# Optimization experiments

Measured on AMD Instinct MI355X. Metric: run time of the kernel, lower is better.

Reference implementation:

```python
import jax, jax.numpy as jnp
import numpy as np
import math

N_FREQ = 128
D_EMB = 64
SLOT_DIM = 256
MLP_HIDDEN = 1024
B, N_SLOTS, N_FEAT = 32, 128, 4096
SIN_DIM = 1 + 2 * N_FREQ
EPS_LN = 1e-5


def _lin_init(key, dout, din):
    k1, k2 = jax.random.split(key)
    s = 1.0 / np.sqrt(din)
    w = jax.random.uniform(k1, (dout, din), minval=-s, maxval=s, dtype=jnp.float32)
    b = jax.random.uniform(k2, (dout,), minval=-s, maxval=s, dtype=jnp.float32)
    return w, b


def setup_inputs() -> dict:
    key = jax.random.key(0)
    ks = jax.random.split(key, 20)
    inp = {}
    # four TimeDepWeight heads: (prefix, d_out, d_in)
    heads = [("q", SLOT_DIM, SLOT_DIM), ("g", SLOT_DIM, 2 * SLOT_DIM),
             ("f0", MLP_HIDDEN, 2 * SLOT_DIM), ("f1", SLOT_DIM, MLP_HIDDEN)]
    i = 0
    for name, dout, din in heads:
        w0, b0 = _lin_init(ks[i], D_EMB, SIN_DIM)
        w1, b1 = _lin_init(ks[i + 1], D_EMB, D_EMB)
        wp, bp = _lin_init(ks[i + 2], dout * din, D_EMB)
        i += 3
        inp[f"{name}_w0"], inp[f"{name}_b0"] = w0, b0
        inp[f"{name}_w1"], inp[f"{name}_b1"] = w1, b1
        inp[f"{name}_wp"], inp[f"{name}_bp"] = wp, bp
    # LayerNorm affine params (eqx.nn.LayerNorm defaults: weight=1, bias=0)
    inp["lnA_w"] = jnp.ones((SLOT_DIM,), jnp.float32)
    inp["lnA_b"] = jnp.zeros((SLOT_DIM,), jnp.float32)
    inp["lnF_w"] = jnp.ones((SLOT_DIM,), jnp.float32)
    inp["lnF_b"] = jnp.zeros((SLOT_DIM,), jnp.float32)
    inp["t"] = jax.random.uniform(ks[12], (1,), dtype=jnp.float32)
    inp["slots"] = jax.random.normal(ks[13], (B, N_SLOTS, SLOT_DIM), jnp.float32)
    inp["k"] = jax.random.normal(ks[14], (B, N_FEAT, SLOT_DIM), jnp.float32)
    inp["v"] = jax.random.normal(ks[15], (B, N_FEAT, SLOT_DIM), jnp.float32)
    return inp


def _tdw(t, w0, b0, w1, b1, wp, bp, d_out, d_in):
    # Sinusoidal(t) -> 2-layer SiLU MLP -> proj -> [d_out, d_in]
    freqs = (-math.log(10000.0) / N_FREQ) * jnp.arange(N_FREQ, dtype=jnp.float32)
    wt = freqs * t
    emb = jnp.concatenate([t[None], jnp.sin(wt), jnp.cos(wt)])
    h = jax.nn.silu(w0 @ emb + b0)
    h = jax.nn.silu(w1 @ h + b1)
    return (wp @ h + bp).reshape(d_out, d_in)


def _layernorm(x, w, b):
    mu = x.mean(-1, keepdims=True)
    var = ((x - mu) ** 2).mean(-1, keepdims=True)
    return (x - mu) / jnp.sqrt(var + EPS_LN) * w + b


def reference(t, slots, k, v,
              q_w0, q_b0, q_w1, q_b1, q_wp, q_bp,
              g_w0, g_b0, g_w1, g_b1, g_wp, g_bp,
              f0_w0, f0_b0, f0_w1, f0_b1, f0_wp, f0_bp,
              f1_w0, f1_b0, f1_w1, f1_b1, f1_wp, f1_bp,
              lnA_w, lnA_b, lnF_w, lnF_b):
    ts = t[0]
    scale = SLOT_DIM ** (-0.5)
    W_q = _tdw(ts, q_w0, q_b0, q_w1, q_b1, q_wp, q_bp, SLOT_DIM, SLOT_DIM)
    W_gate = _tdw(ts, g_w0, g_b0, g_w1, g_b1, g_wp, g_bp, SLOT_DIM, 2 * SLOT_DIM)
    W_ff0 = _tdw(ts, f0_w0, f0_b0, f0_w1, f0_b1, f0_wp, f0_bp, MLP_HIDDEN, 2 * SLOT_DIM)
    W_ff1 = _tdw(ts, f1_w0, f1_b0, f1_w1, f1_b1, f1_wp, f1_bp, SLOT_DIM, MLP_HIDDEN)

    slots_norm = _layernorm(slots, lnA_w, lnA_b)                  # [B,N,D]
    q = jnp.einsum('bnd,od->bno', slots_norm, W_q)                # [B,N,D]
    att_logits = jnp.einsum('bnd,bmd->bnm', q, k) * scale         # [B,N,M]
    att = jax.nn.softmax(att_logits, axis=1)                      # over slots
    att = att / (att.sum(axis=-1, keepdims=True) + 1e-08)         # renorm over feats
    f_attn = jnp.einsum('bnm,bmd->bnd', att, v)                   # [B,N,D]

    gate_input = jnp.concatenate([slots_norm, f_attn], axis=-1)   # [B,N,2D]
    gate = jax.nn.sigmoid(jnp.einsum('bnd,od->bno', gate_input, W_gate))

    slots_ff = _layernorm(slots, lnF_w, lnF_b)
    ff_input = jnp.concatenate([slots_ff, f_attn], axis=-1)       # [B,N,2D]
    h = jax.nn.relu(jnp.einsum('bnd,od->bno', ff_input, W_ff0))   # [B,N,H]
    g_ff = jnp.einsum('bnd,od->bno', h, W_ff1)                    # [B,N,D]
    return gate * f_attn + g_ff
```

## Files before the change

kernel.cpp:

```cpp
#include <hip/hip_runtime.h>
#include <hip/hip_bf16.h>
#include <cstdint>

typedef unsigned short u16;
typedef unsigned int u32;
typedef __attribute__((ext_vector_type(8))) short short8;
typedef __attribute__((ext_vector_type(4))) float f32x4;

#define TID ((int)threadIdx.x)

__device__ __forceinline__ float b2f(u16 u) { return __uint_as_float(((u32)u) << 16); }
__device__ __forceinline__ u16 f2b(float f) {
    u32 u = __float_as_uint(f);
    u += 0x7fffu + ((u >> 16) & 1u);
    return (u16)(u >> 16);
}
__device__ __forceinline__ float2 upk(u32 u) {
    float2 r;
    r.x = __uint_as_float(u << 16);
    r.y = __uint_as_float(u & 0xffff0000u);
    return r;
}
__device__ __forceinline__ float silu_f(float x) { return x / (1.f + __expf(-x)); }

__device__ __forceinline__ float ldx(const void* p, size_t i, bool bf) {
    float v;
    if (bf) v = b2f(((const u16*)p)[i]);
    else    v = ((const float*)p)[i];
    return v;
}

#define BB 32
#define NN 128
#define DD 256
#define MM 4096
#define HH 1024
#define BN (BB * NN)

#define O_FLAG 0
#define O_H2   8
#define O_S    (O_H2 + 256)
#define O_FAT  (O_S + BN)
#define O_WQT  (O_FAT + BN * DD)
#define O_WGT  (O_WQT + 256 * 256)
#define O_WF0T (O_WGT + 512 * 256)
#define O_WF1T (O_WF0T + 512 * 1024)
#define O_SNA  (O_WF1T + 1024 * 256)
#define O_SNF  (O_SNA + BN * DD)
#define O_Q    (O_SNF + BN * DD)
#define O_H    (O_Q + BN * DD)

__global__ void probe_dtype(const void* lnAw, int* flag) {
    u32 bits = *(const u32*)lnAw;
    *flag = ((bits & 0xFFFFu) == 0x3F80u) ? 1 : 0;
}

__global__ __launch_bounds__(256) void tdw_mlp(
    const void* t,
    const void* qw0, const void* qb0, const void* qw1, const void* qb1,
    const void* gw0, const void* gb0, const void* gw1, const void* gb1,
    const void* f0w0, const void* f0b0, const void* f0w1, const void* f0b1,
    const void* f1w0, const void* f1b0, const void* f1w1, const void* f1b1,
    float* h2out, const int* flagp)
{
    __shared__ float emb[257];
    __shared__ float h1s[256];
    bool bf = (*flagp != 0);
    float tv = ldx(t, 0, bf);
    const float c = -9.210340371976184f / 128.f;
    for (int i = TID; i < 257; i += 256) {
        float val;
        if (i == 0) val = tv;
        else if (i <= 128) val = sinf(c * (float)(i - 1) * tv);
        else val = cosf(c * (float)(i - 129) * tv);
        emb[i] = val;
    }
    __syncthreads();
    int head = TID >> 6, o = TID & 63;
    const void* w0s[4] = {qw0, gw0, f0w0, f1w0};
    const void* b0s[4] = {qb0, gb0, f0b0, f1b0};
    const void* w1s[4] = {qw1, gw1, f0w1, f1w1};
    const void* b1s[4] = {qb1, gb1, f0b1, f1b1};
    float acc = ldx(b0s[head], o, bf);
    if (bf) {
        const u16* w0 = (const u16*)w0s[head];
        for (int j = 0; j < 257; j++) acc += b2f(w0[o * 257 + j]) * emb[j];
    } else {
        const float* w0 = (const float*)w0s[head];
        for (int j = 0; j < 257; j++) acc += w0[o * 257 + j] * emb[j];
    }
    h1s[TID] = silu_f(acc);
    __syncthreads();
    float acc2 = ldx(b1s[head], o, bf);
    if (bf) {
        const u16* w1 = (const u16*)w1s[head];
        for (int j = 0; j < 64; j++) acc2 += b2f(w1[o * 64 + j]) * h1s[head * 64 + j];
    } else {
        const float* w1 = (const float*)w1s[head];
        for (int j = 0; j < 64; j++) acc2 += w1[o * 64 + j] * h1s[head * 64 + j];
    }
    h2out[TID] = silu_f(acc2);
}

__global__ __launch_bounds__(256) void tdw_proj(
    const void* __restrict__ wp, const void* __restrict__ bp,
    const float* __restrict__ h2, float* __restrict__ WT,
    int dout_shift, int din, const int* flagp)
{
    __shared__ float h2s[64];
    bool bf = (*flagp != 0);
    if (TID < 64) h2s[TID] = h2[TID];
    __syncthreads();
    int j = blockIdx.x * 256 + TID;
    int d = j >> dout_shift;
    int o = j & ((1 << dout_shift) - 1);
    long i = (long)o * din + d;
    float acc;
    if (bf) acc = b2f(((const u16*)bp)[i]);
    else    acc = ((const float*)bp)[i];
    if (bf) {
        const uint4* row = (const uint4*)((const u16*)wp + i * 64);
#pragma unroll
        for (int r = 0; r < 8; r++) {
            uint4 u = row[r];
            float2 p;
            p = upk(u.x); acc += p.x * h2s[r * 8 + 0] + p.y * h2s[r * 8 + 1];
            p = upk(u.y); acc += p.x * h2s[r * 8 + 2] + p.y * h2s[r * 8 + 3];
            p = upk(u.z); acc += p.x * h2s[r * 8 + 4] + p.y * h2s[r * 8 + 5];
            p = upk(u.w); acc += p.x * h2s[r * 8 + 6] + p.y * h2s[r * 8 + 7];
        }
    } else {
        const float4* row = (const float4*)((const float*)wp + i * 64);
#pragma unroll
        for (int r = 0; r < 16; r++) {
            float4 u = row[r];
            acc += u.x * h2s[r * 4 + 0] + u.y * h2s[r * 4 + 1]
                 + u.z * h2s[r * 4 + 2] + u.w * h2s[r * 4 + 3];
        }
    }
    WT[j] = acc;
}

__global__ __launch_bounds__(256) void layernorm_k(
    const void* __restrict__ slots,
    const void* lnAw, const void* lnAb, const void* lnFw, const void* lnFb,
    float* __restrict__ snA, float* __restrict__ snF, const int* flagp)
{
    int bn = blockIdx.x;
    bool bf = (*flagp != 0);
    float x;
    if (bf) x = b2f(((const u16*)slots)[(size_t)bn * DD + TID]);
    else    x = ((const float*)slots)[(size_t)bn * DD + TID];
    float s1 = x, s2 = x * x;
    for (int off = 32; off; off >>= 1) {
        s1 += __shfl_down(s1, off, 64);
        s2 += __shfl_down(s2, off, 64);
    }
    __shared__ float r1[4], r2[4];
    __shared__ float mu_s, rs_s;
    if ((TID & 63) == 0) { r1[TID >> 6] = s1; r2[TID >> 6] = s2; }
    __syncthreads();
    if (TID == 0) {
        float a = r1[0] + r1[1] + r1[2] + r1[3];
        float b = r2[0] + r2[1] + r2[2] + r2[3];
        float mu = a * (1.f / 256.f);
        float var = b * (1.f / 256.f) - mu * mu;
        mu_s = mu;
        rs_s = rsqrtf(var + 1e-5f);
    }
    __syncthreads();
    float xh = (x - mu_s) * rs_s;
    snA[(size_t)bn * DD + TID] = xh * ldx(lnAw, TID, bf) + ldx(lnAb, TID, bf);
    snF[(size_t)bn * DD + TID] = xh * ldx(lnFw, TID, bf) + ldx(lnFb, TID, bf);
}

__global__ __launch_bounds__(256) void qproj(
    const float* __restrict__ snA, const float* __restrict__ WqT, u16* __restrict__ qb)
{
    int rb = blockIdx.x;
    __shared__ float sn[8][256];
    for (int idx = TID; idx < 2048; idx += 256)
        sn[idx >> 8][idx & 255] = snA[(size_t)rb * 2048 + idx];
    __syncthreads();
    float acc[8] = {0, 0, 0, 0, 0, 0, 0, 0};
    for (int d = 0; d < 256; d++) {
        float w = WqT[d * 256 + TID];
#pragma unroll
        for (int r = 0; r < 8; r++) acc[r] += sn[r][d] * w;
    }
    for (int r = 0; r < 8; r++) qb[(size_t)(rb * 8 + r) * 256 + TID] = f2b(acc[r]);
}

__global__ __launch_bounds__(256, 2) void attn_mfma(
    const u16* __restrict__ qbG,
    const void* __restrict__ k, const void* __restrict__ v,
    float* __restrict__ fat, float* __restrict__ S, const int* flagp)
{
    const int b = blockIdx.y;
    const int m0 = blockIdx.x * 128;
    const bool bf = (*flagp != 0);
    const int t = TID;
    const int l = t & 63, w = t >> 6;
    const int lg = l >> 4;
    const int ll = l & 15;

    __shared__ alignas(16) u16 AB[128 * 128];
    __shared__ alignas(16) u16 vt[256 * 40];

    u16* qb = AB;
    u16* kb = AB + 8192;

    f32x4 acc[2][8];
#pragma unroll
    for (int s = 0; s < 2; s++)
#pragma unroll
        for (int nt = 0; nt < 8; nt++) acc[s][nt] = {0.f, 0.f, 0.f, 0.f};

    for (int dc = 0; dc < 4; dc++) {
        {
            const u32* qg = (const u32*)qbG + (size_t)b * 128 * 128 + dc * 32;
#pragma unroll
            for (int i = 0; i < 16; i++) {
                int fid = i * 256 + t;
                int n = fid >> 5, dp = fid & 31;
                u32 val = qg[n * 128 + dp];
                *(u32*)((char*)qb + n * 128 + ((dp * 4) ^ ((n & 7) << 4))) = val;
            }
        }
        if (bf) {
            const u32* kg = (const u32*)k + ((size_t)(b * MM + m0)) * 128 + dc * 32;
#pragma unroll
            for (int i = 0; i < 16; i++) {
                int fid = i * 256 + t;
                int mm = fid >> 5, dp = fid & 31;
                u32 val = kg[(size_t)mm * 128 + dp];
                *(u32*)((char*)kb + mm * 128 + ((dp * 4) ^ ((mm & 7) << 4))) = val;
            }
        } else {
            const float4* kg = (const float4*)k + ((size_t)(b * MM + m0)) * 64 + dc * 16;
#pragma unroll
            for (int i = 0; i < 8; i++) {
                int fid = i * 256 + t;
                int mm = fid >> 4, q4 = fid & 15;
                float4 f = kg[(size_t)mm * 64 + q4];
                u32 p0 = ((u32)f2b(f.x)) | ((u32)f2b(f.y) << 16);
                u32 p1 = ((u32)f2b(f.z)) | ((u32)f2b(f.w) << 16);
                char* base = (char*)kb + mm * 128;
                *(u32*)(base + (((q4 * 8) + 0) ^ ((mm & 7) << 4))) = p0;
                *(u32*)(base + (((q4 * 8) + 4) ^ ((mm & 7) << 4))) = p1;
            }
        }
        __syncthreads();
#pragma unroll
        for (int ds = 0; ds < 2; ds++) {
            int doff = ds * 64 + lg * 16;
            short8 bfr[2];
#pragma unroll
            for (int s = 0; s < 2; s++) {
                int mm = w * 32 + s * 16 + ll;
                bfr[s] = *(const short8*)((char*)kb + mm * 128 + (doff ^ ((mm & 7) << 4)));
            }
#pragma unroll
            for (int nt = 0; nt < 8; nt++) {
                int n = nt * 16 + ll;
                short8 af = *(const short8*)((char*)qb + n * 128 + (doff ^ ((n & 7) << 4)));
                acc[0][nt] = __builtin_amdgcn_mfma_f32_16x16x32_bf16(af, bfr[0], acc[0][nt], 0, 0, 0);
                acc[1][nt] = __builtin_amdgcn_mfma_f32_16x16x32_bf16(af, bfr[1], acc[1][nt], 0, 0, 0);
            }
        }
        __syncthreads();
    }

    const float scale = 0.0625f;
#pragma unroll
    for (int s = 0; s < 2; s++) {
        float cm = -1e30f;
#pragma unroll
        for (int nt = 0; nt < 8; nt++)
#pragma unroll
            for (int r = 0; r < 4; r++) cm = fmaxf(cm, acc[s][nt][r]);
        cm = fmaxf(cm, __shfl_xor(cm, 16));
        cm = fmaxf(cm, __shfl_xor(cm, 32));
        float cs = 0.f;
#pragma unroll
        for (int nt = 0; nt < 8; nt++)
#pragma unroll
            for (int r = 0; r < 4; r++) {
                float ev = __expf((acc[s][nt][r] - cm) * scale);
                acc[s][nt][r] = ev;
                cs += ev;
            }
        cs += __shfl_xor(cs, 16);
        cs += __shfl_xor(cs, 32);
        float inv = 1.f / cs;
#pragma unroll
        for (int nt = 0; nt < 8; nt++)
#pragma unroll
            for (int r = 0; r < 4; r++) acc[s][nt][r] *= inv;
    }

    u16* att = AB;
#pragma unroll
    for (int s = 0; s < 2; s++)
#pragma unroll
        for (int nt = 0; nt < 8; nt++)
#pragma unroll
            for (int r = 0; r < 4; r++) {
                int n = nt * 16 + lg * 4 + r;
                int mw = w * 32 + s * 16 + ll;
                *(u16*)((char*)att + n * 256 + ((mw * 2) ^ ((n & 7) << 4))) = f2b(acc[s][nt][r]);
            }
#pragma unroll
    for (int nt = 0; nt < 8; nt++)
#pragma unroll
        for (int r = 0; r < 4; r++) {
            float vsum = acc[0][nt][r] + acc[1][nt][r];
            vsum += __shfl_xor(vsum, 1);
            vsum += __shfl_xor(vsum, 2);
            vsum += __shfl_xor(vsum, 4);
            vsum += __shfl_xor(vsum, 8);
            if (ll == 0) atomicAdd(S + b * NN + nt * 16 + lg * 4 + r, vsum);
        }

    f32x4 accp[8][4];
#pragma unroll
    for (int nt = 0; nt < 8; nt++)
#pragma unroll
        for (int dt = 0; dt < 4; dt++) accp[nt][dt] = {0.f, 0.f, 0.f, 0.f};

    for (int ms = 0; ms < 4; ms++) {
        if (bf) {
            const u32* vg = (const u32*)v + ((size_t)(b * MM + m0 + ms * 32)) * 128;
#pragma unroll
            for (int i = 0; i < 16; i++) {
                int fid = i * 256 + t;
                int mm = fid >> 7, du = fid & 127;
                u32 val = vg[(size_t)mm * 128 + du];
                vt[(du * 2 + 0) * 40 + mm] = (u16)(val & 0xffffu);
                vt[(du * 2 + 1) * 40 + mm] = (u16)(val >> 16);
            }
        } else {
            const float4* vg = (const float4*)v + ((size_t)(b * MM + m0 + ms * 32)) * 64;
#pragma unroll
            for (int i = 0; i < 8; i++) {
                int fid = i * 256 + t;
                int mm = fid >> 6, q4 = fid & 63;
                float4 f = vg[(size_t)mm * 64 + q4];
                vt[(q4 * 4 + 0) * 40 + mm] = f2b(f.x);
                vt[(q4 * 4 + 1) * 40 + mm] = f2b(f.y);
                vt[(q4 * 4 + 2) * 40 + mm] = f2b(f.z);
                vt[(q4 * 4 + 3) * 40 + mm] = f2b(f.w);
            }
        }
        __syncthreads();
        short8 bfr[4];
#pragma unroll
        for (int dt = 0; dt < 4; dt++) {
            int dv = w * 64 + dt * 16 + ll;
            bfr[dt] = *(const short8*)(vt + dv * 40 + lg * 8);
        }
#pragma unroll
        for (int nt = 0; nt < 8; nt++) {
            int n = nt * 16 + ll;
            short8 af = *(const short8*)((char*)att + n * 256 + ((ms * 64 + lg * 16) ^ ((n & 7) << 4)));
#pragma unroll
            for (int dt = 0; dt < 4; dt++)
                accp[nt][dt] = __builtin_amdgcn_mfma_f32_16x16x32_bf16(af, bfr[dt], accp[nt][dt], 0, 0, 0);
        }
        __syncthreads();
    }

    float* fb = fat + ((size_t)b * NN) * DD;
#pragma unroll
    for (int nt = 0; nt < 8; nt++)
#pragma unroll
        for (int dt = 0; dt < 4; dt++)
#pragma unroll
            for (int r = 0; r < 4; r++) {
                int n = nt * 16 + lg * 4 + r;
                int dv = w * 64 + dt * 16 + ll;
                atomicAdd(fb + (size_t)n * DD + dv, accp[nt][dt][r]);
            }
}

__global__ __launch_bounds__(256) void ffa(
    const float* __restrict__ snF, const float* __restrict__ fat, const float* __restrict__ S,
    const float* __restrict__ Wf0T, float* __restrict__ h)
{
    int rb = blockIdx.x;
    __shared__ float fi[8][512];
    __shared__ float rsh[8];
    if (TID < 8) rsh[TID] = 1.f / (S[rb * 8 + TID] + 1e-8f);
    __syncthreads();
    for (int idx = TID; idx < 4096; idx += 256) {
        int r = idx >> 9, dd = idx & 511;
        int bn = rb * 8 + r;
        fi[r][dd] = (dd < 256) ? snF[(size_t)bn * 256 + dd]
                               : fat[(size_t)bn * 256 + dd - 256] * rsh[r];
    }
    __syncthreads();
    float acc[8][4] = {};
    for (int d = 0; d < 512; d++) {
        float w0 = Wf0T[d * 1024 + TID];
        float w1 = Wf0T[d * 1024 + TID + 256];
        float w2 = Wf0T[d * 1024 + TID + 512];
        float w3 = Wf0T[d * 1024 + TID + 768];
#pragma unroll
        for (int r = 0; r < 8; r++) {
            float f = fi[r][d];
            acc[r][0] = fmaf(f, w0, acc[r][0]);
            acc[r][1] = fmaf(f, w1, acc[r][1]);
            acc[r][2] = fmaf(f, w2, acc[r][2]);
            acc[r][3] = fmaf(f, w3, acc[r][3]);
        }
    }
    for (int r = 0; r < 8; r++) {
        size_t base = (size_t)(rb * 8 + r) * 1024;
        h[base + TID] = fmaxf(acc[r][0], 0.f);
        h[base + TID + 256] = fmaxf(acc[r][1], 0.f);
        h[base + TID + 512] = fmaxf(acc[r][2], 0.f);
        h[base + TID + 768] = fmaxf(acc[r][3], 0.f);
    }
}

__global__ __launch_bounds__(256) void ffb(
    const float* __restrict__ snA, const float* __restrict__ fat, const float* __restrict__ S,
    const float* __restrict__ WgT, const float* __restrict__ Wf1T,
    const float* __restrict__ h, void* __restrict__ out, const int* flagp)
{
    int rb = blockIdx.x;
    bool bf = (*flagp != 0);
    __shared__ float gi[8][512];
    __shared__ float hs[8][1024];
    __shared__ float rsh[8];
    if (TID < 8) rsh[TID] = 1.f / (S[rb * 8 + TID] + 1e-8f);
    __syncthreads();
    for (int idx = TID; idx < 4096; idx += 256) {
        int r = idx >> 9, dd = idx & 511;
        int bn = rb * 8 + r;
        gi[r][dd] = (dd < 256) ? snA[(size_t)bn * 256 + dd]
                               : fat[(size_t)bn * 256 + dd - 256] * rsh[r];
    }
    for (int idx = TID; idx < 8192; idx += 256) {
        int r = idx >> 10, dd = idx & 1023;
        hs[r][dd] = h[(size_t)(rb * 8 + r) * 1024 + dd];
    }
    __syncthreads();
    float ag[8] = {0, 0, 0, 0, 0, 0, 0, 0};
    float af[8] = {0, 0, 0, 0, 0, 0, 0, 0};
    for (int d = 0; d < 512; d++) {
        float w = WgT[d * 256 + TID];
#pragma unroll
        for (int r = 0; r < 8; r++) ag[r] = fmaf(gi[r][d], w, ag[r]);
    }
    for (int j = 0; j < 1024; j++) {
        float w = Wf1T[j * 256 + TID];
#pragma unroll
        for (int r = 0; r < 8; r++) af[r] = fmaf(hs[r][j], w, af[r]);
    }
    for (int r = 0; r < 8; r++) {
        int bn = rb * 8 + r;
        float fa = gi[r][256 + TID];
        float g = 1.f / (1.f + __expf(-ag[r]));
        float val = g * fa + af[r];
        if (bf) ((u16*)out)[(size_t)bn * 256 + TID] = f2b(val);
        else    ((float*)out)[(size_t)bn * 256 + TID] = val;
    }
}

extern "C" void kernel_launch(void* const* d_in, const int* in_sizes, int n_in,
                              void* d_out, int out_size, void* d_ws, size_t ws_size,
                              hipStream_t stream)
{
    const void* in[32];
    bool sig_order = (n_in >= 1 && in_sizes[0] == 1);
    for (int i = 0; i < 32; i++) {
        int j = sig_order ? ((i < 28) ? (i + 4) : (i - 28)) : i;
        in[i] = d_in[j];
    }

    const void* qw0 = in[0];  const void* qb0 = in[1];
    const void* qw1 = in[2];  const void* qb1 = in[3];
    const void* qwp = in[4];  const void* qbp = in[5];
    const void* gw0 = in[6];  const void* gb0 = in[7];
    const void* gw1 = in[8];  const void* gb1 = in[9];
    const void* gwp = in[10]; const void* gbp = in[11];
    const void* f0w0 = in[12]; const void* f0b0 = in[13];
    const void* f0w1 = in[14]; const void* f0b1 = in[15];
    const void* f0wp = in[16]; const void* f0bp = in[17];
    const void* f1w0 = in[18]; const void* f1b0 = in[19];
    const void* f1w1 = in[20]; const void* f1b1 = in[21];
    const void* f1wp = in[22]; const void* f1bp = in[23];
    const void* lnAw = in[24]; const void* lnAb = in[25];
    const void* lnFw = in[26]; const void* lnFb = in[27];
    const void* t    = in[28]; const void* slots = in[29];
    const void* kk   = in[30]; const void* vv   = in[31];

    float* F = (float*)d_ws;
    int* flagp = (int*)(F + O_FLAG);

    hipMemsetAsync(F + O_S, 0, (size_t)(BN + BN * DD) * sizeof(float), stream);

    probe_dtype<<<1, 1, 0, stream>>>(lnAw, flagp);

    tdw_mlp<<<1, 256, 0, stream>>>(t, qw0, qb0, qw1, qb1, gw0, gb0, gw1, gb1,
                                   f0w0, f0b0, f0w1, f0b1, f1w0, f1b0, f1w1, f1b1,
                                   F + O_H2, flagp);

    tdw_proj<<<256, 256, 0, stream>>>(qwp, qbp, F + O_H2 + 0, F + O_WQT, 8, 256, flagp);
    tdw_proj<<<512, 256, 0, stream>>>(gwp, gbp, F + O_H2 + 64, F + O_WGT, 8, 512, flagp);
    tdw_proj<<<2048, 256, 0, stream>>>(f0wp, f0bp, F + O_H2 + 128, F + O_WF0T, 10, 512, flagp);
    tdw_proj<<<1024, 256, 0, stream>>>(f1wp, f1bp, F + O_H2 + 192, F + O_WF1T, 8, 1024, flagp);

    layernorm_k<<<BN, 256, 0, stream>>>(slots, lnAw, lnAb, lnFw, lnFb,
                                        F + O_SNA, F + O_SNF, flagp);

    qproj<<<BN / 8, 256, 0, stream>>>(F + O_SNA, F + O_WQT, (u16*)(F + O_Q));

    attn_mfma<<<dim3(MM / 128, BB), 256, 0, stream>>>((const u16*)(F + O_Q), kk, vv,
                                                      F + O_FAT, F + O_S, flagp);

    ffa<<<BN / 8, 256, 0, stream>>>(F + O_SNF, F + O_FAT, F + O_S, F + O_WF0T, F + O_H);

    ffb<<<BN / 8, 256, 0, stream>>>(F + O_SNA, F + O_FAT, F + O_S, F + O_WGT, F + O_WF1T,
                                    F + O_H, d_out, flagp);
}
```

Before: 1.132 ms.

## Replace attention atomics with per-tile partials plus reduction; vectorize FFN smem loads

The attention kernel now writes each M-tile's partial f_attn to its own slice of workspace instead of doing float atomicAdd into one buffer, and a new reduce_fat kernel sums the 32 partials. The memset of the fat buffer is dropped accordingly. The qproj, ffa and ffb kernels load into shared memory with float4 and unroll their inner loops by 4 so shared-memory reads are vectorized. The partial buffer adds 32x the f_attn size in extra writes and reads, which trades atomic contention for bandwidth. It also reuses the workspace at O_H, which ffa later overwrites with h, so the ordering matters.

```diff
diff --git a/kernel.cpp b/kernel.cpp
--- a/kernel.cpp
+++ b/kernel.cpp
@@ -49,6 +49,7 @@
 #define O_SNF  (O_SNA + BN * DD)
 #define O_Q    (O_SNF + BN * DD)
 #define O_H    (O_Q + BN * DD)
+#define O_FATP O_H
 
 __global__ void probe_dtype(const void* lnAw, int* flag) {
     u32 bits = *(const u32*)lnAw;
@@ -179,14 +180,22 @@
 {
     int rb = blockIdx.x;
     __shared__ float sn[8][256];
-    for (int idx = TID; idx < 2048; idx += 256)
-        sn[idx >> 8][idx & 255] = snA[(size_t)rb * 2048 + idx];
+    for (int idx = TID; idx < 512; idx += 256) {
+        int r = idx >> 6, q4 = idx & 63;
+        *(float4*)&sn[r][q4 * 4] = *(const float4*)(snA + (size_t)rb * 2048 + r * 256 + q4 * 4);
+    }
     __syncthreads();
     float acc[8] = {0, 0, 0, 0, 0, 0, 0, 0};
-    for (int d = 0; d < 256; d++) {
-        float w = WqT[d * 256 + TID];
-#pragma unroll
-        for (int r = 0; r < 8; r++) acc[r] += sn[r][d] * w;
+    for (int d = 0; d < 256; d += 4) {
+        float w0 = WqT[(d + 0) * 256 + TID];
+        float w1 = WqT[(d + 1) * 256 + TID];
+        float w2 = WqT[(d + 2) * 256 + TID];
+        float w3 = WqT[(d + 3) * 256 + TID];
+#pragma unroll
+        for (int r = 0; r < 8; r++) {
+            float4 s4 = *(const float4*)&sn[r][d];
+            acc[r] = fmaf(s4.x, w0, fmaf(s4.y, w1, fmaf(s4.z, w2, fmaf(s4.w, w3, acc[r]))));
+        }
     }
     for (int r = 0; r < 8; r++) qb[(size_t)(rb * 8 + r) * 256 + TID] = f2b(acc[r]);
 }
@@ -194,10 +203,11 @@
 __global__ __launch_bounds__(256, 2) void attn_mfma(
     const u16* __restrict__ qbG,
     const void* __restrict__ k, const void* __restrict__ v,
-    float* __restrict__ fat, float* __restrict__ S, const int* flagp)
+    float* __restrict__ fatP, float* __restrict__ S, const int* flagp)
 {
     const int b = blockIdx.y;
-    const int m0 = blockIdx.x * 128;
+    const int mt = blockIdx.x;
+    const int m0 = mt * 128;
     const bool bf = (*flagp != 0);
     const int t = TID;
     const int l = t & 63, w = t >> 6;
@@ -370,7 +380,7 @@
         __syncthreads();
     }
 
-    float* fb = fat + ((size_t)b * NN) * DD;
+    float* fp = fatP + ((size_t)mt * BN + (size_t)b * NN) * DD;
 #pragma unroll
     for (int nt = 0; nt < 8; nt++)
 #pragma unroll
@@ -379,8 +389,21 @@
             for (int r = 0; r < 4; r++) {
                 int n = nt * 16 + lg * 4 + r;
                 int dv = w * 64 + dt * 16 + ll;
-                atomicAdd(fb + (size_t)n * DD + dv, accp[nt][dt][r]);
-            }
+                fp[(size_t)n * DD + dv] = accp[nt][dt][r];
+            }
+}
+
+__global__ __launch_bounds__(256) void reduce_fat(
+    const float* __restrict__ fatP, float* __restrict__ fat)
+{
+    size_t i = ((size_t)blockIdx.x * 256 + TID) * 4;
+    float4 a = *(const float4*)(fatP + i);
+#pragma unroll
+    for (int mt = 1; mt < 32; mt++) {
+        float4 bb = *(const float4*)(fatP + (size_t)mt * (size_t)BN * DD + i);
+        a.x += bb.x; a.y += bb.y; a.z += bb.z; a.w += bb.w;
+    }
+    *(float4*)(fat + i) = a;
 }
 
 __global__ __launch_bounds__(256) void ffa(
@@ -392,26 +415,37 @@
     __shared__ float rsh[8];
     if (TID < 8) rsh[TID] = 1.f / (S[rb * 8 + TID] + 1e-8f);
     __syncthreads();
-    for (int idx = TID; idx < 4096; idx += 256) {
-        int r = idx >> 9, dd = idx & 511;
-        int bn = rb * 8 + r;
-        fi[r][dd] = (dd < 256) ? snF[(size_t)bn * 256 + dd]
-                               : fat[(size_t)bn * 256 + dd - 256] * rsh[r];
+    for (int idx = TID; idx < 1024; idx += 256) {
+        int r = idx >> 7, q4 = idx & 127;
+        size_t bn = (size_t)rb * 8 + r;
+        float4 val;
+        if (q4 < 64) val = *(const float4*)(snF + bn * 256 + q4 * 4);
+        else {
+            val = *(const float4*)(fat + bn * 256 + (q4 - 64) * 4);
+            float s = rsh[r];
+            val.x *= s; val.y *= s; val.z *= s; val.w *= s;
+        }
+        *(float4*)&fi[r][q4 * 4] = val;
     }
     __syncthreads();
     float acc[8][4] = {};
-    for (int d = 0; d < 512; d++) {
-        float w0 = Wf0T[d * 1024 + TID];
-        float w1 = Wf0T[d * 1024 + TID + 256];
-        float w2 = Wf0T[d * 1024 + TID + 512];
-        float w3 = Wf0T[d * 1024 + TID + 768];
+    for (int d = 0; d < 512; d += 4) {
+        float w[4][4];
+#pragma unroll
+        for (int kk2 = 0; kk2 < 4; kk2++) {
+            const float* wp_ = Wf0T + (size_t)(d + kk2) * 1024 + TID;
+            w[kk2][0] = wp_[0];   w[kk2][1] = wp_[256];
+            w[kk2][2] = wp_[512]; w[kk2][3] = wp_[768];
+        }
 #pragma unroll
         for (int r = 0; r < 8; r++) {
-            float f = fi[r][d];
-            acc[r][0] = fmaf(f, w0, acc[r][0]);
-            acc[r][1] = fmaf(f, w1, acc[r][1]);
-            acc[r][2] = fmaf(f, w2, acc[r][2]);
-            acc[r][3] = fmaf(f, w3, acc[r][3]);
+            float4 f = *(const float4*)&fi[r][d];
+            float fv[4] = {f.x, f.y, f.z, f.w};
+#pragma unroll
+            for (int kk2 = 0; kk2 < 4; kk2++)
+#pragma unroll
+                for (int c = 0; c < 4; c++)
+                    acc[r][c] = fmaf(fv[kk2], w[kk2][c], acc[r][c]);
         }
     }
     for (int r = 0; r < 8; r++) {
@@ -435,28 +469,46 @@
     __shared__ float rsh[8];
     if (TID < 8) rsh[TID] = 1.f / (S[rb * 8 + TID] + 1e-8f);
     __syncthreads();
-    for (int idx = TID; idx < 4096; idx += 256) {
-        int r = idx >> 9, dd = idx & 511;
-        int bn = rb * 8 + r;
-        gi[r][dd] = (dd < 256) ? snA[(size_t)bn * 256 + dd]
-                               : fat[(size_t)bn * 256 + dd - 256] * rsh[r];
-    }
-    for (int idx = TID; idx < 8192; idx += 256) {
-        int r = idx >> 10, dd = idx & 1023;
-        hs[r][dd] = h[(size_t)(rb * 8 + r) * 1024 + dd];
+    for (int idx = TID; idx < 1024; idx += 256) {
+        int r = idx >> 7, q4 = idx & 127;
+        size_t bn = (size_t)rb * 8 + r;
+        float4 val;
+        if (q4 < 64) val = *(const float4*)(snA + bn * 256 + q4 * 4);
+        else {
+            val = *(const float4*)(fat + bn * 256 + (q4 - 64) * 4);
+            float s = rsh[r];
+            val.x *= s; val.y *= s; val.z *= s; val.w *= s;
+        }
+        *(float4*)&gi[r][q4 * 4] = val;
+    }
+    for (int idx = TID; idx < 2048; idx += 256) {
+        int r = idx >> 8, q4 = idx & 255;
+        *(float4*)&hs[r][q4 * 4] = *(const float4*)(h + (size_t)(rb * 8 + r) * 1024 + q4 * 4);
     }
     __syncthreads();
     float ag[8] = {0, 0, 0, 0, 0, 0, 0, 0};
     float af[8] = {0, 0, 0, 0, 0, 0, 0, 0};
-    for (int d = 0; d < 512; d++) {
-        float w = WgT[d * 256 + TID];
-#pragma unroll
-        for (int r = 0; r < 8; r++) ag[r] = fmaf(gi[r][d], w, ag[r]);
-    }
-    for (int j = 0; j < 1024; j++) {
-        float w = Wf1T[j * 256 + TID];
-#pragma unroll
-        for (int r = 0; r < 8; r++) af[r] = fmaf(hs[r][j], w, af[r]);
+    for (int d = 0; d < 512; d += 4) {
+        float w0 = WgT[(d + 0) * 256 + TID];
+        float w1 = WgT[(d + 1) * 256 + TID];
+        float w2 = WgT[(d + 2) * 256 + TID];
+        float w3 = WgT[(d + 3) * 256 + TID];
+#pragma unroll
+        for (int r = 0; r < 8; r++) {
+            float4 g = *(const float4*)&gi[r][d];
+            ag[r] = fmaf(g.x, w0, fmaf(g.y, w1, fmaf(g.z, w2, fmaf(g.w, w3, ag[r]))));
+        }
+    }
+    for (int j = 0; j < 1024; j += 4) {
+        float w0 = Wf1T[(j + 0) * 256 + TID];
+        float w1 = Wf1T[(j + 1) * 256 + TID];
+        float w2 = Wf1T[(j + 2) * 256 + TID];
+        float w3 = Wf1T[(j + 3) * 256 + TID];
+#pragma unroll
+        for (int r = 0; r < 8; r++) {
+            float4 hv = *(const float4*)&hs[r][j];
+            af[r] = fmaf(hv.x, w0, fmaf(hv.y, w1, fmaf(hv.z, w2, fmaf(hv.w, w3, af[r]))));
+        }
     }
     for (int r = 0; r < 8; r++) {
         int bn = rb * 8 + r;
@@ -499,7 +551,7 @@
     float* F = (float*)d_ws;
     int* flagp = (int*)(F + O_FLAG);
 
-    hipMemsetAsync(F + O_S, 0, (size_t)(BN + BN * DD) * sizeof(float), stream);
+    hipMemsetAsync(F + O_S, 0, (size_t)BN * sizeof(float), stream);
 
     probe_dtype<<<1, 1, 0, stream>>>(lnAw, flagp);
 
@@ -518,7 +570,9 @@
     qproj<<<BN / 8, 256, 0, stream>>>(F + O_SNA, F + O_WQT, (u16*)(F + O_Q));
 
     attn_mfma<<<dim3(MM / 128, BB), 256, 0, stream>>>((const u16*)(F + O_Q), kk, vv,
-                                                      F + O_FAT, F + O_S, flagp);
+                                                      F + O_FATP, F + O_S, flagp);
+
+    reduce_fat<<<BN * DD / 1024, 256, 0, stream>>>(F + O_FATP, F + O_FAT);
 
     ffa<<<BN / 8, 256, 0, stream>>>(F + O_SNF, F + O_FAT, F + O_S, F + O_WF0T, F + O_H);
 
```

Measured after the change: 1.012 ms. 10.6% less time.
